# Performance work log

Measured on AMD Instinct MI355X. Metric: run time of the kernel, lower is better.

Reference implementation:

```python
import jax, jax.numpy as jnp
import numpy as np

NS = 8          # neighborhood_size
PAD = NS // 2   # pad_size
BW = 0.5        # band_width
EPS_NORM = 1e-12  # F.normalize eps
EPS = 1e-5


def setup_inputs() -> dict:
    key = jax.random.key(0)
    k1, k2, k3, k4, k5 = jax.random.split(key, 5)
    N, C, H, W, D = 2, 48, 64, 64, 64
    S = 10  # num_samples
    x = jax.random.normal(k1, (N, C, H, W, D), dtype=jnp.float32)
    y = jax.random.normal(k2, (N, C, H, W, D), dtype=jnp.float32)
    # torch.randint(pad, H-pad) -> indices in [4, 60)
    h_indices = jax.random.randint(k3, (S,), PAD, H - PAD)
    w_indices = jax.random.randint(k4, (S,), PAD, W - PAD)
    d_indices = jax.random.randint(k5, (S,), PAD, D - PAD)
    return {"x": x, "y": y, "h_indices": h_indices,
            "w_indices": w_indices, "d_indices": d_indices}


def _contextual_loss_3d(x, y, h_idx, w_idx, d_idx):
    N, C = x.shape[0], x.shape[1]

    def slice_neigh(a, hi, wi, di):
        # 8x8x8 cube around (hi, wi, di) -> (N, C, NS, NS, NS)
        return jax.lax.dynamic_slice(
            a, (0, 0, hi - PAD, wi - PAD, di - PAD), (N, C, NS, NS, NS))

    def per_sample(hi, wi, di):
        xn = slice_neigh(x, hi, wi, di).reshape(N, C, -1)  # (N, C, M), M=512
        yn = slice_neigh(y, hi, wi, di).reshape(N, C, -1)
        y_mu = yn.mean(axis=(0, 2), keepdims=True)          # (1, C, 1)
        xc = xn - y_mu
        yc = yn - y_mu
        # F.normalize(p=2, dim=1): divide by max(||.||, eps)
        xc = xc / jnp.maximum(jnp.linalg.norm(xc, axis=1, keepdims=True), EPS_NORM)
        yc = yc / jnp.maximum(jnp.linalg.norm(yc, axis=1, keepdims=True), EPS_NORM)
        dist = 1.0 - jnp.einsum('ncm,ncp->nmp', xc, yc)     # (N, M, M)
        dist_min = dist.min(axis=2, keepdims=True)
        dist_tilde = dist / (dist_min + EPS)
        cx = jax.nn.softmax((1.0 - dist_tilde) / BW, axis=2)
        cx = cx.max(axis=1).mean(axis=1)                    # (N,)
        return jnp.mean(-jnp.log(cx + EPS))

    losses = jax.vmap(per_sample)(h_idx, w_idx, d_idx)      # (S,)
    return losses.mean()


def reference(x, y, h_indices, w_indices, d_indices):
    return _contextual_loss_3d(x, y, h_indices, w_indices, d_indices)
```

## Files before the change

### kernel.cpp

```cpp
#include <hip/hip_runtime.h>
#include <hip/hip_bf16.h>
#include <math.h>

#define S_    10
#define C_    48
#define HWD   64
#define M_    512
#define PADK  4
#define PAIRS 20

#define OFF_GY  0
#define OFF_GX  491520
#define OFF_MU  983040
#define OFF_CNT (OFF_MU + 480)
#define OFF_ALL (OFF_CNT + 20)
#define OFF_PL  (OFF_ALL + 1)
#define ZERO_N  (20 + 1 + 20)
#define OFF_YK  983584
#define OFF_XK  (OFF_YK + 327680)
#define OFF_PM  (OFF_XK + 327680)

typedef __attribute__((ext_vector_type(8))) short bf16x8;
typedef __attribute__((ext_vector_type(4))) float f32x4;

__device__ __forceinline__ int gidx(int n, int c, int h, int w, int d) {
  return (((n * C_ + c) * HWD + h) * HWD + w) * HWD + d;
}

__device__ __forceinline__ unsigned short f2bf(float f) {
  unsigned u = __float_as_uint(f);
  u += 0x7FFFu + ((u >> 16) & 1u);
  return (unsigned short)(u >> 16);
}

__device__ __forceinline__ int fidx(int m, int c) {
  return ((m >> 4) << 10) + ((c >> 5) << 9) + (((c >> 3) & 3) << 7) +
         ((m & 15) << 3) + (c & 7);
}

__global__ void k_gather(const float* __restrict__ x, const float* __restrict__ y,
                         const int* __restrict__ hi, const int* __restrict__ wi,
                         const int* __restrict__ di, float* __restrict__ ws) {
  int b = blockIdx.x, t = threadIdx.x;
  int lane = t & 63, wv = t >> 6;
  __shared__ float red[4];
  if (b == 0 && t < ZERO_N) ws[OFF_CNT + t] = 0.f;
  int which = b >= 480;
  int r = which ? b - 480 : b;
  int s = r / C_, c = r % C_;
  const float* src = which ? x : y;
  int h0 = hi[s] - PADK, w0 = wi[s] - PADK, d0 = di[s] - PADK;
  float* dst = ws + (which ? OFF_GX : OFF_GY) + (s * 96 + 2 * c) * 512;
  float sum = 0.f;
#pragma unroll
  for (int j = 0; j < 4; ++j) {
    int i = t + 256 * j;
    int n = i >> 9, m = i & 511;
    float v = src[gidx(n, c, h0 + (m >> 6), w0 + ((m >> 3) & 7), d0 + (m & 7))];
    dst[n * 512 + m] = v;
    sum += v;
  }
  if (!which) {
#pragma unroll
    for (int off = 32; off; off >>= 1) sum += __shfl_xor(sum, off);
    if (lane == 0) red[wv] = sum;
    __syncthreads();
    if (t == 0)
      ws[OFF_MU + s * C_ + c] =
          (red[0] + red[1] + red[2] + red[3]) * (1.0f / 1024.0f);
  }
}

__global__ void k_nc(float* __restrict__ ws) {
  int g = blockIdx.x * 256 + threadIdx.x;
  int col = g >> 2;
  int q = threadIdx.x & 3;
  int which = col >= 10240;
  int cix = which ? col - 10240 : col;
  int pair = cix >> 9, m = cix & 511;
  int s = pair >> 1, n = pair & 1;
  const float* base = ws + (which ? OFF_GX : OFF_GY) + (s * 96 + n) * 512 + m;
  const float* mus = ws + OFF_MU + s * C_;
  int c0 = q * 12;
  float v[12], ss = 0.f;
#pragma unroll
  for (int j = 0; j < 12; ++j) {
    v[j] = base[(c0 + j) * 1024] - mus[c0 + j];
    ss += v[j] * v[j];
  }
  ss += __shfl_xor(ss, 1);
  ss += __shfl_xor(ss, 2);
  float sc = 1.0f / fmaxf(sqrtf(ss), 1e-12f);
  unsigned short* dstk = (unsigned short*)(ws + (which ? OFF_XK : OFF_YK)) +
                         pair * 32768;
#pragma unroll
  for (int j = 0; j < 12; ++j) dstk[fidx(m, c0 + j)] = f2bf(v[j] * sc);
  if (q == 3) {
#pragma unroll
    for (int c = 48; c < 64; ++c) dstk[fidx(m, c)] = 0;
  }
}

__global__ __launch_bounds__(64, 2) void k_mm(float* __restrict__ ws) {
  int b = blockIdx.x;
  int pair = b >> 5, slab = b & 31;
  int lane = threadIdx.x;

  const unsigned short* xf =
      (const unsigned short*)(ws + OFF_XK) + pair * 32768;
  const unsigned short* yf =
      (const unsigned short*)(ws + OFF_YK) + pair * 32768;

  bf16x8 a0 = *(const bf16x8*)(xf + slab * 1024 + lane * 8);
  bf16x8 a1 = *(const bf16x8*)(xf + slab * 1024 + 512 + lane * 8);

  f32x4 d[32];
#pragma unroll
  for (int ct = 0; ct < 32; ++ct) {
    bf16x8 b0 = *(const bf16x8*)(yf + ct * 1024 + lane * 8);
    bf16x8 b1 = *(const bf16x8*)(yf + ct * 1024 + 512 + lane * 8);
    f32x4 z = {0.f, 0.f, 0.f, 0.f};
    f32x4 dd = __builtin_amdgcn_mfma_f32_16x16x32_bf16(a0, b0, z, 0, 0, 0);
    d[ct] = __builtin_amdgcn_mfma_f32_16x16x32_bf16(a1, b1, dd, 0, 0, 0);
  }

  float am0 = -3.4e38f, am1 = -3.4e38f, am2 = -3.4e38f, am3 = -3.4e38f;
#pragma unroll
  for (int ct = 0; ct < 32; ++ct) {
    am0 = fmaxf(am0, d[ct][0]); am1 = fmaxf(am1, d[ct][1]);
    am2 = fmaxf(am2, d[ct][2]); am3 = fmaxf(am3, d[ct][3]);
  }
#pragma unroll
  for (int off = 1; off < 16; off <<= 1) {
    am0 = fmaxf(am0, __shfl_xor(am0, off));
    am1 = fmaxf(am1, __shfl_xor(am1, off));
    am2 = fmaxf(am2, __shfl_xor(am2, off));
    am3 = fmaxf(am3, __shfl_xor(am3, off));
  }
  float inv0 = 2.f / ((1.f - am0) + 1e-5f), c20 = 2.f - inv0;
  float inv1 = 2.f / ((1.f - am1) + 1e-5f), c21 = 2.f - inv1;
  float inv2 = 2.f / ((1.f - am2) + 1e-5f), c22 = 2.f - inv2;
  float inv3 = 2.f / ((1.f - am3) + 1e-5f), c23 = 2.f - inv3;
  float sm0 = 0.f, sm1 = 0.f, sm2 = 0.f, sm3 = 0.f;
#pragma unroll
  for (int ct = 0; ct < 32; ++ct) {
    float e0 = __expf(fmaf(d[ct][0], inv0, c20));
    float e1 = __expf(fmaf(d[ct][1], inv1, c21));
    float e2 = __expf(fmaf(d[ct][2], inv2, c22));
    float e3 = __expf(fmaf(d[ct][3], inv3, c23));
    d[ct][0] = e0; d[ct][1] = e1; d[ct][2] = e2; d[ct][3] = e3;
    sm0 += e0; sm1 += e1; sm2 += e2; sm3 += e3;
  }
#pragma unroll
  for (int off = 1; off < 16; off <<= 1) {
    sm0 += __shfl_xor(sm0, off); sm1 += __shfl_xor(sm1, off);
    sm2 += __shfl_xor(sm2, off); sm3 += __shfl_xor(sm3, off);
  }
  float rs0 = 1.f / sm0, rs1 = 1.f / sm1, rs2 = 1.f / sm2, rs3 = 1.f / sm3;
  float* pm = ws + OFF_PM + (pair * 32 + slab) * M_;
#pragma unroll
  for (int ct = 0; ct < 32; ++ct) {
    float cc = fmaxf(fmaxf(d[ct][0] * rs0, d[ct][1] * rs1),
                     fmaxf(d[ct][2] * rs2, d[ct][3] * rs3));
    cc = fmaxf(cc, __shfl_xor(cc, 16));
    cc = fmaxf(cc, __shfl_xor(cc, 32));
    if (lane < 16) pm[ct * 16 + lane] = cc;
  }
}

__global__ void k_final(float* __restrict__ ws, float* __restrict__ out) {
  int pair = blockIdx.x;
  int t = threadIdx.x, lane = t & 63, wv = t >> 6;
  __shared__ float red[4];
  __shared__ int lastflag;
  const float* pm = ws + OFF_PM + pair * 32 * M_;

  float m0 = 0.f, m1 = 0.f;
  for (int s = 0; s < 32; ++s) {
    m0 = fmaxf(m0, pm[s * M_ + t]);
    m1 = fmaxf(m1, pm[s * M_ + t + 256]);
  }
  float sum = m0 + m1;
#pragma unroll
  for (int off = 32; off; off >>= 1) sum += __shfl_xor(sum, off);
  if (lane == 0) red[wv] = sum;
  if (t == 0) lastflag = 0;
  __syncthreads();
  if (t == 0) {
    float tot = red[0] + red[1] + red[2] + red[3];
    float loss = -logf(tot * (1.0f / 512.0f) + 1e-5f);
    atomicExch((unsigned*)(ws + OFF_PL) + pair, __float_as_uint(loss));
    __threadfence();
    unsigned dct = atomicAdd((unsigned*)(ws + OFF_ALL), 1u);
    if (dct == PAIRS - 1) lastflag = 1;
  }
  __syncthreads();
  if (lastflag && t < 32) {
    float v = (t < PAIRS)
                  ? __uint_as_float(atomicOr((unsigned*)(ws + OFF_PL) + t, 0u))
                  : 0.f;
#pragma unroll
    for (int off = 16; off; off >>= 1) v += __shfl_xor(v, off);
    if (t == 0) out[0] = v * (1.0f / (float)PAIRS);
  }
}

extern "C" void kernel_launch(void* const* d_in, const int* in_sizes, int n_in,
                              void* d_out, int out_size, void* d_ws, size_t ws_size,
                              hipStream_t stream) {
  const float* x = (const float*)d_in[0];
  const float* y = (const float*)d_in[1];
  const int* hi = (const int*)d_in[2];
  const int* wi = (const int*)d_in[3];
  const int* di = (const int*)d_in[4];
  float* ws = (float*)d_ws;
  float* out = (float*)d_out;

  k_gather<<<960, 256, 0, stream>>>(x, y, hi, wi, di, ws);
  k_nc<<<320, 256, 0, stream>>>(ws);
  k_mm<<<PAIRS * 32, 64, 0, stream>>>(ws);
  k_final<<<PAIRS, 256, 0, stream>>>(ws, out);
}
```

Baseline: 32.13 us.

## Fuse x gather and normalization directly into the MFMA kernel

Removes the x-side gather into workspace and the x-side normalize/bf16 pack pass. Instead, each k_mm wave reads its 16 x columns straight from global memory, centers them with the y mean, normalizes, and builds the bf16 A fragments in registers. This halves the gather and normalize grids and cuts workspace traffic. The cost is strided, uncoalesced global loads inside the matmul kernel and extra register pressure there.

Result: slower. 33.21 us (+3.4%).

```diff
diff --git a/kernel.cpp b/kernel.cpp
--- a/kernel.cpp
+++ b/kernel.cpp
@@ -8,17 +8,16 @@
 #define M_    512
 #define PADK  4
 #define PAIRS 20
+#define CSTRIDE (HWD * HWD * HWD)
 
 #define OFF_GY  0
-#define OFF_GX  491520
-#define OFF_MU  983040
+#define OFF_MU  491520
 #define OFF_CNT (OFF_MU + 480)
 #define OFF_ALL (OFF_CNT + 20)
 #define OFF_PL  (OFF_ALL + 1)
 #define ZERO_N  (20 + 1 + 20)
-#define OFF_YK  983584
-#define OFF_XK  (OFF_YK + 327680)
-#define OFF_PM  (OFF_XK + 327680)
+#define OFF_YK  492032
+#define OFF_PM  (OFF_YK + 327680)
 
 typedef __attribute__((ext_vector_type(8))) short bf16x8;
 typedef __attribute__((ext_vector_type(4))) float f32x4;
@@ -38,48 +37,41 @@
          ((m & 15) << 3) + (c & 7);
 }
 
-__global__ void k_gather(const float* __restrict__ x, const float* __restrict__ y,
-                         const int* __restrict__ hi, const int* __restrict__ wi,
-                         const int* __restrict__ di, float* __restrict__ ws) {
+__global__ void k_gather(const float* __restrict__ y, const int* __restrict__ hi,
+                         const int* __restrict__ wi, const int* __restrict__ di,
+                         float* __restrict__ ws) {
   int b = blockIdx.x, t = threadIdx.x;
   int lane = t & 63, wv = t >> 6;
   __shared__ float red[4];
   if (b == 0 && t < ZERO_N) ws[OFF_CNT + t] = 0.f;
-  int which = b >= 480;
-  int r = which ? b - 480 : b;
-  int s = r / C_, c = r % C_;
-  const float* src = which ? x : y;
+  int s = b / C_, c = b % C_;
   int h0 = hi[s] - PADK, w0 = wi[s] - PADK, d0 = di[s] - PADK;
-  float* dst = ws + (which ? OFF_GX : OFF_GY) + (s * 96 + 2 * c) * 512;
+  float* dst = ws + OFF_GY + (s * 96 + 2 * c) * 512;
   float sum = 0.f;
 #pragma unroll
   for (int j = 0; j < 4; ++j) {
     int i = t + 256 * j;
     int n = i >> 9, m = i & 511;
-    float v = src[gidx(n, c, h0 + (m >> 6), w0 + ((m >> 3) & 7), d0 + (m & 7))];
+    float v = y[gidx(n, c, h0 + (m >> 6), w0 + ((m >> 3) & 7), d0 + (m & 7))];
     dst[n * 512 + m] = v;
     sum += v;
   }
-  if (!which) {
-#pragma unroll
-    for (int off = 32; off; off >>= 1) sum += __shfl_xor(sum, off);
-    if (lane == 0) red[wv] = sum;
-    __syncthreads();
-    if (t == 0)
-      ws[OFF_MU + s * C_ + c] =
-          (red[0] + red[1] + red[2] + red[3]) * (1.0f / 1024.0f);
-  }
+#pragma unroll
+  for (int off = 32; off; off >>= 1) sum += __shfl_xor(sum, off);
+  if (lane == 0) red[wv] = sum;
+  __syncthreads();
+  if (t == 0)
+    ws[OFF_MU + s * C_ + c] =
+        (red[0] + red[1] + red[2] + red[3]) * (1.0f / 1024.0f);
 }
 
 __global__ void k_nc(float* __restrict__ ws) {
   int g = blockIdx.x * 256 + threadIdx.x;
   int col = g >> 2;
   int q = threadIdx.x & 3;
-  int which = col >= 10240;
-  int cix = which ? col - 10240 : col;
-  int pair = cix >> 9, m = cix & 511;
+  int pair = col >> 9, m = col & 511;
   int s = pair >> 1, n = pair & 1;
-  const float* base = ws + (which ? OFF_GX : OFF_GY) + (s * 96 + n) * 512 + m;
+  const float* base = ws + OFF_GY + (s * 96 + n) * 512 + m;
   const float* mus = ws + OFF_MU + s * C_;
   int c0 = q * 12;
   float v[12], ss = 0.f;
@@ -91,8 +83,7 @@
   ss += __shfl_xor(ss, 1);
   ss += __shfl_xor(ss, 2);
   float sc = 1.0f / fmaxf(sqrtf(ss), 1e-12f);
-  unsigned short* dstk = (unsigned short*)(ws + (which ? OFF_XK : OFF_YK)) +
-                         pair * 32768;
+  unsigned short* dstk = (unsigned short*)(ws + OFF_YK) + pair * 32768;
 #pragma unroll
   for (int j = 0; j < 12; ++j) dstk[fidx(m, c0 + j)] = f2bf(v[j] * sc);
   if (q == 3) {
@@ -101,19 +92,49 @@
   }
 }
 
-__global__ __launch_bounds__(64, 2) void k_mm(float* __restrict__ ws) {
+__global__ __launch_bounds__(64, 2) void k_mm(const float* __restrict__ x,
+                                              const int* __restrict__ hi,
+                                              const int* __restrict__ wi,
+                                              const int* __restrict__ di,
+                                              float* __restrict__ ws) {
   int b = blockIdx.x;
   int pair = b >> 5, slab = b & 31;
+  int s = pair >> 1, n = pair & 1;
   int lane = threadIdx.x;
-
-  const unsigned short* xf =
-      (const unsigned short*)(ws + OFF_XK) + pair * 32768;
-  const unsigned short* yf =
-      (const unsigned short*)(ws + OFF_YK) + pair * 32768;
-
-  bf16x8 a0 = *(const bf16x8*)(xf + slab * 1024 + lane * 8);
-  bf16x8 a1 = *(const bf16x8*)(xf + slab * 1024 + 512 + lane * 8);
-
+  int r16 = lane & 15, kg = lane >> 4;
+
+  int h0 = hi[s] - PADK, w0 = wi[s] - PADK, d0 = di[s] - PADK;
+  int m = slab * 16 + r16;
+  int xb = gidx(n, 0, h0 + (m >> 6), w0 + ((m >> 3) & 7), d0 + (m & 7));
+  const float* mus = ws + OFF_MU + s * C_;
+  int c0 = kg * 8, c1 = 32 + kg * 8;
+  float v0[8], v1[8], ss = 0.f;
+#pragma unroll
+  for (int j = 0; j < 8; ++j) {
+    v0[j] = x[xb + (c0 + j) * CSTRIDE] - mus[c0 + j];
+    ss += v0[j] * v0[j];
+  }
+  if (kg < 2) {
+#pragma unroll
+    for (int j = 0; j < 8; ++j) {
+      v1[j] = x[xb + (c1 + j) * CSTRIDE] - mus[c1 + j];
+      ss += v1[j] * v1[j];
+    }
+  } else {
+#pragma unroll
+    for (int j = 0; j < 8; ++j) v1[j] = 0.f;
+  }
+  ss += __shfl_xor(ss, 16);
+  ss += __shfl_xor(ss, 32);
+  float sc = 1.0f / fmaxf(sqrtf(ss), 1e-12f);
+  bf16x8 a0, a1;
+#pragma unroll
+  for (int j = 0; j < 8; ++j) {
+    a0[j] = (short)f2bf(v0[j] * sc);
+    a1[j] = (short)f2bf(v1[j] * sc);
+  }
+
+  const unsigned short* yf = (const unsigned short*)(ws + OFF_YK) + pair * 32768;
   f32x4 d[32];
 #pragma unroll
   for (int ct = 0; ct < 32; ++ct) {
@@ -176,9 +197,9 @@
   const float* pm = ws + OFF_PM + pair * 32 * M_;
 
   float m0 = 0.f, m1 = 0.f;
-  for (int s = 0; s < 32; ++s) {
-    m0 = fmaxf(m0, pm[s * M_ + t]);
-    m1 = fmaxf(m1, pm[s * M_ + t + 256]);
+  for (int s2 = 0; s2 < 32; ++s2) {
+    m0 = fmaxf(m0, pm[s2 * M_ + t]);
+    m1 = fmaxf(m1, pm[s2 * M_ + t + 256]);
   }
   float sum = m0 + m1;
 #pragma unroll
@@ -216,8 +237,8 @@
   float* ws = (float*)d_ws;
   float* out = (float*)d_out;
 
-  k_gather<<<960, 256, 0, stream>>>(x, y, hi, wi, di, ws);
-  k_nc<<<320, 256, 0, stream>>>(ws);
-  k_mm<<<PAIRS * 32, 64, 0, stream>>>(ws);
+  k_gather<<<S_ * C_, 256, 0, stream>>>(y, hi, wi, di, ws);
+  k_nc<<<160, 256, 0, stream>>>(ws);
+  k_mm<<<PAIRS * 32, 64, 0, stream>>>(x, hi, wi, di, ws);
   k_final<<<PAIRS, 256, 0, stream>>>(ws, out);
 }
```
